# Kernel optimization log

Measured on AMD Instinct MI355X. Metric: run time of the kernel, lower is better.

Reference implementation:

```python
import jax, jax.numpy as jnp
import numpy as np

# ---- GridEncoder config (torch-ngp semantics) ----
NUM_LEVELS = 16
LEVEL_DIM = 8
BASE_RES = 16
LOG2_HASH = 19
PER_LEVEL_SCALE = 2.0
BOUNDS = 10.0
N_POINTS = 200000
FEAT = NUM_LEVELS * LEVEL_DIM        # 128
MLP_W = 256
OUT_DIM = 1024                        # image(512) + affordance(512)
_PRIMES = (1, 2654435761, 805459861)  # instant-NGP spatial hash primes


def _level_meta():
    # replicates torch-ngp GridEncoder.__init__ offset computation
    max_params = 1 << LOG2_HASH
    metas, offset = [], 0
    for l in range(NUM_LEVELS):
        scale = BASE_RES * (PER_LEVEL_SCALE ** l) - 1.0
        res = int(np.ceil(scale)) + 1
        p = min(max_params, (res + 1) ** 3)      # align_corners=False -> res+1
        p = int(np.ceil(p / 8) * 8)
        metas.append((scale, res, p, offset))
        offset += p
    return metas, offset

LEVEL_META, TOTAL_PARAMS = _level_meta()
_CORNERS = np.array([[(c >> d) & 1 for d in range(3)] for c in range(8)], dtype=np.float32)  # [8,3]


def grid_encode(x01, table):
    """x01: [N,3] in [0,1]; table: [TOTAL_PARAMS, LEVEL_DIM]. Returns [N, FEAT]."""
    cf = jnp.asarray(_CORNERS)                        # float corners [8,3]
    ci = jnp.asarray(_CORNERS.astype(np.uint32))      # int corners
    outs = []
    for scale, res, hsize, off in LEVEL_META:
        pos = x01 * scale + 0.5                       # align_corners=False offset
        pg = jnp.floor(pos)
        frac = pos - pg                               # [N,3]
        # trilinear weights for the 8 corners: prod_d (frac or 1-frac)
        w = jnp.prod(frac[:, None, :] * cf + (1.0 - frac[:, None, :]) * (1.0 - cf), axis=-1)  # [N,8]
        coords = pg.astype(jnp.uint32)[:, None, :] + ci                                        # [N,8,3]
        if (res + 1) ** 3 <= hsize:
            # dense level: strided linear index over (res+1)^3 grid
            idx = (coords[..., 0]
                   + coords[..., 1] * np.uint32(res + 1)
                   + coords[..., 2] * np.uint32((res + 1) ** 2))
        else:
            # hashed level: xor of coordinate * prime (uint32 wraparound)
            idx = ((coords[..., 0] * jnp.uint32(_PRIMES[0]))
                   ^ (coords[..., 1] * jnp.uint32(_PRIMES[1]))
                   ^ (coords[..., 2] * jnp.uint32(_PRIMES[2])))
        idx = (idx % jnp.uint32(hsize)).astype(jnp.int32) + off
        feats = table[idx]                             # gather [N,8,LEVEL_DIM]
        outs.append(jnp.einsum('nc,ncd->nd', w, feats))
    return jnp.concatenate(outs, axis=-1)              # [N, FEAT]


def setup_inputs() -> dict:
    key = jax.random.key(0)
    ks = jax.random.split(key, 16)
    def nrm(k, shape):
        return jax.random.normal(k, shape, dtype=jnp.float32) * 0.02
    inp = {
        'x': jax.random.uniform(ks[0], (N_POINTS, 3), jnp.float32, -BOUNDS, BOUNDS),
        'affordance_values': jax.random.uniform(ks[1], (N_POINTS,), jnp.float32),
        # instant-NGP init: U(-1e-4, 1e-4)
        'grid_table': jax.random.uniform(ks[2], (TOTAL_PARAMS, LEVEL_DIM), jnp.float32, -1e-4, 1e-4),
        'Wa': nrm(ks[3], (FEAT, 1)), 'ba': jnp.zeros((FEAT,), jnp.float32),
        'Wq': nrm(ks[4], (FEAT, FEAT)), 'bq': jnp.zeros((FEAT,), jnp.float32),
        'Wk': nrm(ks[5], (FEAT, FEAT)), 'bk': jnp.zeros((FEAT,), jnp.float32),
        'Wv': nrm(ks[6], (FEAT, FEAT)), 'bv': jnp.zeros((FEAT,), jnp.float32),
        'Wo': nrm(ks[7], (FEAT, FEAT)), 'bo': jnp.zeros((FEAT,), jnp.float32),
        'W1': nrm(ks[8], (MLP_W, FEAT)), 'b1': jnp.zeros((MLP_W,), jnp.float32),
        'W2': nrm(ks[9], (MLP_W, MLP_W)), 'b2': jnp.zeros((MLP_W,), jnp.float32),
        'W3': nrm(ks[10], (OUT_DIM, MLP_W)), 'b3': jnp.zeros((OUT_DIM,), jnp.float32),
    }
    return inp


def reference(x, affordance_values, grid_table, Wa, ba, Wq, bq, Wk, bk, Wv, bv, Wo, bo,
              W1, b1, W2, b2, W3, b3):
    # normalize coords to [0,1] using fixed bounds (+-BOUNDS)
    bounded = (x + BOUNDS) / (2.0 * BOUNDS)
    # GridEncoder.forward maps inputs from [-bound, bound] -> [0,1] with bound=1.0
    x01 = (bounded + 1.0) / 2.0
    grid_hash = grid_encode(x01, grid_table)                      # [N, FEAT]
    aff_emb = affordance_values[:, None] @ Wa.T + ba              # Linear(1, FEAT)
    comb = grid_hash + aff_emb                                    # [N, FEAT]
    # MultiheadAttention with seq_len=1: each head's softmax is over a single
    # key, so attn weight == 1 regardless of q/k -> output = out_proj(v_proj(x)).
    v = comb @ Wv.T + bv
    attn = v @ Wo.T + bo
    # MLP head: [Linear+ReLU] x hidden_depth, then Linear to OUT_DIM
    h = jax.nn.relu(attn @ W1.T + b1)
    h = jax.nn.relu(h @ W2.T + b2)
    out = h @ W3.T + b3                                           # [N, 1024]
    return out[:, :512], out[:, 512:]                             # image, affordance latents
```

## Files before the change

kernel.cpp:

```cpp
#include <hip/hip_runtime.h>
#include <stdint.h>

typedef __attribute__((ext_vector_type(8))) short bf16x8;
typedef __attribute__((ext_vector_type(4))) float f32x4;

__device__ __forceinline__ ushort f2bf(float f) {
    uint32_t u = __float_as_uint(f);
    return (ushort)((u + 0x7FFFu + ((u >> 16) & 1u)) >> 16);
}

__device__ const int d_level_off[16] = {
    0, 4920, 40864, 315496, 839784, 1364072, 1888360, 2412648,
    2936936, 3461224, 3985512, 4509800, 5034088, 5558376, 6082664, 6606952
};

__global__ __launch_bounds__(256) void grid_encode_kernel(
    const float* __restrict__ x, const float* __restrict__ aff,
    const float* __restrict__ table, const float* __restrict__ Wa,
    const float* __restrict__ ba, ushort* __restrict__ comb,
    int npts, int npts_pad)
{
    int t = blockIdx.x * 256 + threadIdx.x;
    int n = t >> 4;
    if (n >= npts_pad) return;
    int l = t & 15;
    int fb = l * 8;
    uint32_t pk[4] = {0u, 0u, 0u, 0u};

    if (n < npts) {
        float scale = (float)((16 << l) - 1);
        float fr[3];
        uint32_t cc[3];
        #pragma unroll
        for (int d = 0; d < 3; ++d) {
            float b   = (x[n * 3 + d] + 10.0f) / 20.0f;
            float x01 = (b + 1.0f) * 0.5f;
            float pos = x01 * scale + 0.5f;
            float pg  = floorf(pos);
            fr[d] = pos - pg;
            cc[d] = (uint32_t)(int)pg;
        }

        const bool dense = (l < 3);
        const uint32_t s1 = (uint32_t)(16 << l) + 1u;
        const uint32_t s2 = s1 * s1;
        const int off = d_level_off[l];

        float fa[8] = {0.f, 0.f, 0.f, 0.f, 0.f, 0.f, 0.f, 0.f};
        #pragma unroll
        for (int c = 0; c < 8; ++c) {
            uint32_t cx = cc[0] + (uint32_t)(c & 1);
            uint32_t cy = cc[1] + (uint32_t)((c >> 1) & 1);
            uint32_t cz = cc[2] + (uint32_t)((c >> 2) & 1);
            float w = ((c & 1) ? fr[0] : 1.0f - fr[0])
                    * ((c & 2) ? fr[1] : 1.0f - fr[1])
                    * ((c & 4) ? fr[2] : 1.0f - fr[2]);
            uint32_t idx;
            if (dense) idx = cx + cy * s1 + cz * s2;
            else       idx = (cx ^ (cy * 2654435761u) ^ (cz * 805459861u)) & 0x7FFFFu;
            const float4* p = (const float4*)(table + (size_t)(idx + (uint32_t)off) * 8u);
            float4 t0 = p[0];
            float4 t1 = p[1];
            fa[0] = fmaf(w, t0.x, fa[0]);
            fa[1] = fmaf(w, t0.y, fa[1]);
            fa[2] = fmaf(w, t0.z, fa[2]);
            fa[3] = fmaf(w, t0.w, fa[3]);
            fa[4] = fmaf(w, t1.x, fa[4]);
            fa[5] = fmaf(w, t1.y, fa[5]);
            fa[6] = fmaf(w, t1.z, fa[6]);
            fa[7] = fmaf(w, t1.w, fa[7]);
        }

        float av = aff[n];
        #pragma unroll
        for (int j = 0; j < 4; ++j) {
            float o0 = fa[2 * j]     + av * Wa[fb + 2 * j]     + ba[fb + 2 * j];
            float o1 = fa[2 * j + 1] + av * Wa[fb + 2 * j + 1] + ba[fb + 2 * j + 1];
            pk[j] = (uint32_t)f2bf(o0) | ((uint32_t)f2bf(o1) << 16);
        }
    }
    *(uint4*)(comb + (size_t)n * 128 + fb) = make_uint4(pk[0], pk[1], pk[2], pk[3]);
}

__global__ void small_mm(const float* __restrict__ A, const float* __restrict__ B,
                         float* __restrict__ C, int Mo, int No, int Ko)
{
    int gid = blockIdx.x * 256 + threadIdx.x;
    if (gid >= Mo * No) return;
    int j = gid / No, k = gid % No;
    float s = 0.f;
    for (int i = 0; i < Ko; ++i) s = fmaf(A[j * Ko + i], B[i * No + k], s);
    C[gid] = s;
}

__global__ void small_mv(const float* __restrict__ A, const float* __restrict__ v,
                         const float* __restrict__ b0, float* __restrict__ out,
                         int Mo, int Ko)
{
    int j = blockIdx.x * 256 + threadIdx.x;
    if (j >= Mo) return;
    float s = b0[j];
    for (int i = 0; i < Ko; ++i) s = fmaf(A[j * Ko + i], v[i], s);
    out[j] = s;
}

__global__ void f32_to_bf16_kernel(const float* __restrict__ in,
                                   ushort* __restrict__ out, int n)
{
    int i = blockIdx.x * 256 + threadIdx.x;
    if (i < n) out[i] = f2bf(in[i]);
}

__global__ __launch_bounds__(256) void gemm_mfma(
    const ushort* __restrict__ A, const ushort* __restrict__ B,
    const float* __restrict__ bias, void* __restrict__ Cv,
    int N, int K, int mode, int npts)
{
    __shared__ ushort As[128 * 64];
    __shared__ ushort Bs[128 * 64];

    const int tid  = threadIdx.x;
    const int bn   = blockIdx.x;
    const int bm   = blockIdx.y;
    const int lane = tid & 63;
    const int wave = tid >> 6;
    const int wm   = wave >> 1, wn = wave & 1;
    const int l15  = lane & 15, lhi = lane >> 4;

    f32x4 acc[4][4] = {};

    int rowc[4], kcc[4];
    #pragma unroll
    for (int i = 0; i < 4; ++i) {
        int c = tid + i * 256;
        rowc[i] = c >> 3;
        kcc[i]  = ((c & 7) ^ (rowc[i] & 7)) * 8;
    }

    for (int k0 = 0; k0 < K; k0 += 64) {
        #pragma unroll
        for (int i = 0; i < 4; ++i) {
            int c = tid + i * 256;
            const ushort* ga = A + (size_t)(bm * 128 + rowc[i]) * (size_t)K + (k0 + kcc[i]);
            __builtin_amdgcn_global_load_lds(
                (const __attribute__((address_space(1))) uint32_t*)ga,
                (__attribute__((address_space(3))) uint32_t*)&As[c * 8], 16, 0, 0);
            const ushort* gb = B + (size_t)(bn * 128 + rowc[i]) * (size_t)K + (k0 + kcc[i]);
            __builtin_amdgcn_global_load_lds(
                (const __attribute__((address_space(1))) uint32_t*)gb,
                (__attribute__((address_space(3))) uint32_t*)&Bs[c * 8], 16, 0, 0);
        }
        __syncthreads();

        #pragma unroll
        for (int kk = 0; kk < 64; kk += 32) {
            bf16x8 a[4], b[4];
            int ks = (kk >> 3) + lhi;
            #pragma unroll
            for (int f = 0; f < 4; ++f) {
                int ra = wm * 64 + f * 16 + l15;
                a[f] = *(const bf16x8*)&As[ra * 64 + ((ks ^ (ra & 7)) << 3)];
                int rb = wn * 64 + f * 16 + l15;
                b[f] = *(const bf16x8*)&Bs[rb * 64 + ((ks ^ (rb & 7)) << 3)];
            }
            #pragma unroll
            for (int i = 0; i < 4; ++i)
                #pragma unroll
                for (int j = 0; j < 4; ++j)
                    acc[i][j] = __builtin_amdgcn_mfma_f32_16x16x32_bf16(
                        a[i], b[j], acc[i][j], 0, 0, 0);
        }
        __syncthreads();
    }

    float bb[4];
    #pragma unroll
    for (int j = 0; j < 4; ++j)
        bb[j] = bias[bn * 128 + wn * 64 + j * 16 + l15];

    if (mode == 1) {
        ushort* Cb = (ushort*)Cv;
        #pragma unroll
        for (int i = 0; i < 4; ++i) {
            #pragma unroll
            for (int r = 0; r < 4; ++r) {
                int m = bm * 128 + wm * 64 + i * 16 + lhi * 4 + r;
                ushort* dst = Cb + (size_t)m * N + bn * 128 + wn * 64 + l15;
                #pragma unroll
                for (int j = 0; j < 4; ++j) {
                    float v = acc[i][j][r] + bb[j];
                    dst[j * 16] = f2bf(fmaxf(v, 0.f));
                }
            }
        }
    } else {
        float* out = (float*)Cv;
        const int nh = (bn >= 4);
        float* plane = out + (nh ? (size_t)npts * 512 : 0);
        const int ncol = bn * 128 - nh * 512 + wn * 64 + l15;
        #pragma unroll
        for (int i = 0; i < 4; ++i) {
            #pragma unroll
            for (int r = 0; r < 4; ++r) {
                int m = bm * 128 + wm * 64 + i * 16 + lhi * 4 + r;
                if (m < npts) {
                    float* dst = plane + (size_t)m * 512 + ncol;
                    #pragma unroll
                    for (int j = 0; j < 4; ++j)
                        dst[j * 16] = acc[i][j][r] + bb[j];
                }
            }
        }
    }
}

extern "C" void kernel_launch(void* const* d_in, const int* in_sizes, int n_in,
                              void* d_out, int out_size, void* d_ws, size_t ws_size,
                              hipStream_t stream)
{
    const float* x     = (const float*)d_in[0];
    const float* aff   = (const float*)d_in[1];
    const float* table = (const float*)d_in[2];
    const float* Wa    = (const float*)d_in[3];
    const float* ba    = (const float*)d_in[4];
    const float* Wv    = (const float*)d_in[9];
    const float* bv    = (const float*)d_in[10];
    const float* Wo    = (const float*)d_in[11];
    const float* bo    = (const float*)d_in[12];
    const float* W1    = (const float*)d_in[13];
    const float* b1    = (const float*)d_in[14];
    const float* W2    = (const float*)d_in[15];
    const float* b2    = (const float*)d_in[16];
    const float* W3    = (const float*)d_in[17];
    const float* b3    = (const float*)d_in[18];
    const int npts = in_sizes[0] / 3;
    const int mb = (npts + 127) / 128;
    const int npts_pad = mb * 128;

    float* ws = (float*)d_ws;
    float*  Wvo  = ws;
    float*  bvo  = ws + 16384;
    float*  W1c  = ws + 16512;
    float*  b1c  = ws + 49280;
    ushort* W1cb = (ushort*)(ws + 49536);
    ushort* W2b  = (ushort*)(ws + 65920);
    ushort* W3b  = (ushort*)(ws + 98688);
    ushort* comb = (ushort*)(ws + 229760);
    ushort* h1   = comb + (size_t)npts_pad * 128;
    ushort* h2   = h1   + (size_t)npts_pad * 256;

    small_mm<<<64, 256, 0, stream>>>(Wo, Wv, Wvo, 128, 128, 128);
    small_mv<<<1, 256, 0, stream>>>(Wo, bv, bo, bvo, 128, 128);
    small_mm<<<128, 256, 0, stream>>>(W1, Wvo, W1c, 256, 128, 128);
    small_mv<<<1, 256, 0, stream>>>(W1, bvo, b1, b1c, 256, 128);

    f32_to_bf16_kernel<<<128, 256, 0, stream>>>(W1c, W1cb, 32768);
    f32_to_bf16_kernel<<<256, 256, 0, stream>>>(W2, W2b, 65536);
    f32_to_bf16_kernel<<<1024, 256, 0, stream>>>(W3, W3b, 262144);

    grid_encode_kernel<<<(npts_pad * 16) / 256, 256, 0, stream>>>(
        x, aff, table, Wa, ba, comb, npts, npts_pad);

    gemm_mfma<<<dim3(2, mb), 256, 0, stream>>>(comb, W1cb, b1c, h1, 256, 128, 1, npts);
    gemm_mfma<<<dim3(2, mb), 256, 0, stream>>>(h1, W2b, b2, h2, 256, 256, 1, npts);
    gemm_mfma<<<dim3(8, mb), 256, 0, stream>>>(h2, W3b, b3, d_out, 1024, 256, 2, npts);
}
```

Baseline: 1.566 ms.

## Fuse three MLP GEMMs into one kernel keeping hidden activations in LDS

Replaces the three separate MFMA GEMM launches with a single fused kernel per 128-row tile. The kernel loads the combined features into LDS, computes layers 1 and 2 with the hidden activations held in swizzled LDS buffers, then produces the 1024-wide output in four 256-column chunks. This removes the global-memory round trips for the h1/h2 intermediates and two launches. Weights are now read directly from global memory (L2) per wave rather than staged through LDS, and 128KB of LDS per block limits occupancy.

```diff
diff --git a/kernel.cpp b/kernel.cpp
--- a/kernel.cpp
+++ b/kernel.cpp
@@ -111,98 +111,117 @@
     if (i < n) out[i] = f2bf(in[i]);
 }
 
-__global__ __launch_bounds__(256) void gemm_mfma(
-    const ushort* __restrict__ A, const ushort* __restrict__ B,
-    const float* __restrict__ bias, void* __restrict__ Cv,
-    int N, int K, int mode, int npts)
-{
-    __shared__ ushort As[128 * 64];
-    __shared__ ushort Bs[128 * 64];
+
+template<int K>
+__device__ __forceinline__ void mfma_stage(
+    const ushort* As,
+    const ushort* __restrict__ W,
+    int wm, int wn, int l15, int lhi, f32x4 (&acc)[4][4])
+{
+    #pragma unroll
+    for (int kstep = 0; kstep < K / 32; ++kstep) {
+        bf16x8 a[4], b[4];
+        const int ks = kstep * 4 + lhi;
+        #pragma unroll
+        for (int f = 0; f < 4; ++f) {
+            const int ra = wm * 64 + f * 16 + l15;
+            a[f] = *(const bf16x8*)&As[ra * K + ((ks ^ (ra & 7)) << 3)];
+            const int rb = wn * 64 + f * 16 + l15;
+            b[f] = *(const bf16x8*)&W[(size_t)rb * K + kstep * 32 + lhi * 8];
+        }
+        #pragma unroll
+        for (int i = 0; i < 4; ++i)
+            #pragma unroll
+            for (int j = 0; j < 4; ++j)
+                acc[i][j] = __builtin_amdgcn_mfma_f32_16x16x32_bf16(
+                    a[i], b[j], acc[i][j], 0, 0, 0);
+    }
+}
+
+__device__ __forceinline__ void store_h_lds(
+    ushort* H, const f32x4 (&acc)[4][4], const float* __restrict__ bias,
+    int wm, int wn, int l15, int lhi)
+{
+    float bb[4];
+    #pragma unroll
+    for (int j = 0; j < 4; ++j) bb[j] = bias[wn * 64 + j * 16 + l15];
+    #pragma unroll
+    for (int i = 0; i < 4; ++i)
+        #pragma unroll
+        for (int r = 0; r < 4; ++r) {
+            const int m = wm * 64 + i * 16 + lhi * 4 + r;
+            #pragma unroll
+            for (int j = 0; j < 4; ++j) {
+                const int n = wn * 64 + j * 16 + l15;
+                const int slot = n >> 3;
+                H[m * 256 + (((slot ^ (m & 7)) << 3) | (n & 7))] =
+                    f2bf(fmaxf(acc[i][j][r] + bb[j], 0.f));
+            }
+        }
+}
+
+__global__ __launch_bounds__(512, 2) void fused_mlp(
+    const ushort* __restrict__ comb,
+    const ushort* __restrict__ W1,
+    const float*  __restrict__ b1,
+    const ushort* __restrict__ W2,
+    const float*  __restrict__ b2,
+    const ushort* __restrict__ W3,
+    const float*  __restrict__ b3,
+    float* __restrict__ out, int npts)
+{
+    __shared__ ushort hA[128 * 256];
+    __shared__ ushort hB[128 * 256];
 
     const int tid  = threadIdx.x;
-    const int bn   = blockIdx.x;
-    const int bm   = blockIdx.y;
+    const int bm   = blockIdx.x;
     const int lane = tid & 63;
     const int wave = tid >> 6;
-    const int wm   = wave >> 1, wn = wave & 1;
+    const int wm   = wave >> 2, wn = wave & 3;
     const int l15  = lane & 15, lhi = lane >> 4;
 
-    f32x4 acc[4][4] = {};
-
-    int rowc[4], kcc[4];
     #pragma unroll
     for (int i = 0; i < 4; ++i) {
-        int c = tid + i * 256;
-        rowc[i] = c >> 3;
-        kcc[i]  = ((c & 7) ^ (rowc[i] & 7)) * 8;
-    }
-
-    for (int k0 = 0; k0 < K; k0 += 64) {
-        #pragma unroll
-        for (int i = 0; i < 4; ++i) {
-            int c = tid + i * 256;
-            const ushort* ga = A + (size_t)(bm * 128 + rowc[i]) * (size_t)K + (k0 + kcc[i]);
-            __builtin_amdgcn_global_load_lds(
-                (const __attribute__((address_space(1))) uint32_t*)ga,
-                (__attribute__((address_space(3))) uint32_t*)&As[c * 8], 16, 0, 0);
-            const ushort* gb = B + (size_t)(bn * 128 + rowc[i]) * (size_t)K + (k0 + kcc[i]);
-            __builtin_amdgcn_global_load_lds(
-                (const __attribute__((address_space(1))) uint32_t*)gb,
-                (__attribute__((address_space(3))) uint32_t*)&Bs[c * 8], 16, 0, 0);
-        }
-        __syncthreads();
-
-        #pragma unroll
-        for (int kk = 0; kk < 64; kk += 32) {
-            bf16x8 a[4], b[4];
-            int ks = (kk >> 3) + lhi;
-            #pragma unroll
-            for (int f = 0; f < 4; ++f) {
-                int ra = wm * 64 + f * 16 + l15;
-                a[f] = *(const bf16x8*)&As[ra * 64 + ((ks ^ (ra & 7)) << 3)];
-                int rb = wn * 64 + f * 16 + l15;
-                b[f] = *(const bf16x8*)&Bs[rb * 64 + ((ks ^ (rb & 7)) << 3)];
-            }
-            #pragma unroll
-            for (int i = 0; i < 4; ++i)
-                #pragma unroll
-                for (int j = 0; j < 4; ++j)
-                    acc[i][j] = __builtin_amdgcn_mfma_f32_16x16x32_bf16(
-                        a[i], b[j], acc[i][j], 0, 0, 0);
-        }
-        __syncthreads();
-    }
-
-    float bb[4];
-    #pragma unroll
-    for (int j = 0; j < 4; ++j)
-        bb[j] = bias[bn * 128 + wn * 64 + j * 16 + l15];
-
-    if (mode == 1) {
-        ushort* Cb = (ushort*)Cv;
-        #pragma unroll
-        for (int i = 0; i < 4; ++i) {
+        const int c = tid + i * 512;
+        const int r = c >> 4, s = c & 15;
+        const ushort* g = comb + (size_t)(bm * 128 + r) * 128 + ((s ^ (r & 7)) * 8);
+        __builtin_amdgcn_global_load_lds(
+            (const __attribute__((address_space(1))) uint32_t*)g,
+            (__attribute__((address_space(3))) uint32_t*)&hB[c * 8], 16, 0, 0);
+    }
+    __syncthreads();
+
+    {
+        f32x4 acc[4][4] = {};
+        mfma_stage<128>(hB, W1, wm, wn, l15, lhi, acc);
+        store_h_lds(hA, acc, b1, wm, wn, l15, lhi);
+    }
+    __syncthreads();
+
+    {
+        f32x4 acc[4][4] = {};
+        mfma_stage<256>(hA, W2, wm, wn, l15, lhi, acc);
+        store_h_lds(hB, acc, b2, wm, wn, l15, lhi);
+    }
+    __syncthreads();
+
+    #pragma unroll 1
+    for (int ch = 0; ch < 4; ++ch) {
+        f32x4 acc[4][4] = {};
+        mfma_stage<256>(hB, W3 + (size_t)ch * 256 * 256, wm, wn, l15, lhi, acc);
+
+        float bb[4];
+        #pragma unroll
+        for (int j = 0; j < 4; ++j) bb[j] = b3[ch * 256 + wn * 64 + j * 16 + l15];
+
+        const int colg = ch * 256 + wn * 64 + l15;
+        float* plane   = out + ((ch >= 2) ? (size_t)npts * 512 : 0);
+        const int ncol = colg - ((ch >= 2) ? 512 : 0);
+        #pragma unroll
+        for (int i = 0; i < 4; ++i)
             #pragma unroll
             for (int r = 0; r < 4; ++r) {
-                int m = bm * 128 + wm * 64 + i * 16 + lhi * 4 + r;
-                ushort* dst = Cb + (size_t)m * N + bn * 128 + wn * 64 + l15;
-                #pragma unroll
-                for (int j = 0; j < 4; ++j) {
-                    float v = acc[i][j][r] + bb[j];
-                    dst[j * 16] = f2bf(fmaxf(v, 0.f));
-                }
-            }
-        }
-    } else {
-        float* out = (float*)Cv;
-        const int nh = (bn >= 4);
-        float* plane = out + (nh ? (size_t)npts * 512 : 0);
-        const int ncol = bn * 128 - nh * 512 + wn * 64 + l15;
-        #pragma unroll
-        for (int i = 0; i < 4; ++i) {
-            #pragma unroll
-            for (int r = 0; r < 4; ++r) {
-                int m = bm * 128 + wm * 64 + i * 16 + lhi * 4 + r;
+                const int m = bm * 128 + wm * 64 + i * 16 + lhi * 4 + r;
                 if (m < npts) {
                     float* dst = plane + (size_t)m * 512 + ncol;
                     #pragma unroll
@@ -210,7 +229,6 @@
                         dst[j * 16] = acc[i][j][r] + bb[j];
                 }
             }
-        }
     }
 }
 
@@ -246,8 +264,6 @@
     ushort* W2b  = (ushort*)(ws + 65920);
     ushort* W3b  = (ushort*)(ws + 98688);
     ushort* comb = (ushort*)(ws + 229760);
-    ushort* h1   = comb + (size_t)npts_pad * 128;
-    ushort* h2   = h1   + (size_t)npts_pad * 256;
 
     small_mm<<<64, 256, 0, stream>>>(Wo, Wv, Wvo, 128, 128, 128);
     small_mv<<<1, 256, 0, stream>>>(Wo, bv, bo, bvo, 128, 128);
@@ -261,7 +277,6 @@
     grid_encode_kernel<<<(npts_pad * 16) / 256, 256, 0, stream>>>(
         x, aff, table, Wa, ba, comb, npts, npts_pad);
 
-    gemm_mfma<<<dim3(2, mb), 256, 0, stream>>>(comb, W1cb, b1c, h1, 256, 128, 1, npts);
-    gemm_mfma<<<dim3(2, mb), 256, 0, stream>>>(h1, W2b, b2, h2, 256, 256, 1, npts);
-    gemm_mfma<<<dim3(8, mb), 256, 0, stream>>>(h2, W3b, b3, d_out, 1024, 256, 2, npts);
-}
+    fused_mlp<<<mb, 512, 0, stream>>>(comb, W1cb, b1c, W2b, b2, W3b, b3,
+                                      (float*)d_out, npts);
+}
```

Result: slower. 1.666 ms (+6.3%).
